# Performance work log

Hardware: AMD Instinct MI355X
Metric: run time of the kernel (lower is better)

The kernel has to match this reference:

```python
import jax, jax.numpy as jnp
import numpy as np

B = 256          # block_size
IN_BLOCKS = 16
OUT_BLOCKS = 16
BATCH, SEQ = 4, 2048


def setup_inputs() -> dict:
    key = jax.random.key(0)
    k1, k2, k3 = jax.random.split(key, 3)
    x = jax.random.normal(k1, (BATCH, SEQ, IN_BLOCKS * B), dtype=jnp.float32)
    c = jax.random.normal(k2, (OUT_BLOCKS, IN_BLOCKS, B), dtype=jnp.float32) * 0.01
    bias = jnp.zeros((OUT_BLOCKS * B,), dtype=jnp.float32)
    return {"x": x, "c": c, "bias": bias}


def reference(x, c, bias):
    # x: (batch, seq, in_features); c: (J, I, B); bias: (J*B,)
    batch, seq, in_f = x.shape
    J, I, Bsz = c.shape
    x_blocks = x.reshape(batch * seq, I, Bsz)            # (N, I, B)
    # FFT in float32 (matches circulant_matvec_fft internals)
    fft_c = jnp.fft.rfft(c.astype(jnp.float32), axis=-1)         # (J, I, F)
    fft_x = jnp.fft.rfft(x_blocks.astype(jnp.float32), axis=-1)  # (N, I, F)
    # y[n,j] = sum_i C_{j,i} x[n,i]  -> frequency-domain multiply + reduce over i
    fft_y = jnp.einsum('jif,nif->njf', fft_c, fft_x)              # (N, J, F)
    y_blocks = jnp.fft.irfft(fft_y, n=Bsz, axis=-1)               # (N, J, B)
    y = y_blocks.reshape(batch * seq, J * Bsz).astype(x.dtype) + bias
    return y.reshape(batch, seq, J * Bsz)
```

## Files before the change

kernel.cpp:

```cpp
#include <hip/hip_runtime.h>

typedef unsigned int uint;
typedef unsigned short ushort;
typedef __attribute__((ext_vector_type(8))) short  short8;
typedef __attribute__((ext_vector_type(8))) unsigned short u16x8;
typedef __attribute__((ext_vector_type(4))) float  f32x4;

__device__ __forceinline__ ushort f2b(float f) {
    uint u = __float_as_uint(f);
    u += 0x7FFFu + ((u >> 16) & 1u);
    return (ushort)(u >> 16);
}

__device__ __forceinline__ void async16(const void* g, void* l) {
    __builtin_amdgcn_global_load_lds(
        (const __attribute__((address_space(1))) void*)g,
        (__attribute__((address_space(3))) void*)l,
        16, 0, 0);
}

__global__ __launch_bounds__(256) void expand_w(const float* __restrict__ c,
                                                ushort* __restrict__ Wt) {
    const int j = blockIdx.x >> 4;
    const int i = blockIdx.x & 15;
    __shared__ ushort crev2[512];
    const float* cs = c + (size_t)(j * 16 + i) * 256;
    const int t = threadIdx.x;
    {
        ushort b = f2b(cs[(256 - t) & 255]);
        crev2[t] = b;
        crev2[t + 256] = b;
    }
    __syncthreads();
    const int tr = t >> 5;
    const int tm = (t & 31) * 8;
    for (int rb = 0; rb < 256; rb += 8) {
        const int k = rb + tr;
        u16x8 v;
#pragma unroll
        for (int u = 0; u < 8; ++u) v[u] = crev2[tm + u - k + 256];
        *(u16x8*)&Wt[(size_t)(j * 256 + k) * 4096 + i * 256 + tm] = v;
    }
}

__global__ __launch_bounds__(256) void conv_x(const float4* __restrict__ x,
                                              u16x8* __restrict__ xb, int n8) {
    int idx = blockIdx.x * blockDim.x + threadIdx.x;
    const int stride = gridDim.x * blockDim.x;
    for (; idx < n8; idx += stride) {
        float4 a = x[idx * 2];
        float4 b = x[idx * 2 + 1];
        u16x8 o;
        o[0] = f2b(a.x); o[1] = f2b(a.y); o[2] = f2b(a.z); o[3] = f2b(a.w);
        o[4] = f2b(b.x); o[5] = f2b(b.y); o[6] = f2b(b.z); o[7] = f2b(b.w);
        xb[idx] = o;
    }
}

#define BAR()   __builtin_amdgcn_s_barrier()
#define LGKM0() asm volatile("s_waitcnt lgkmcnt(0)" ::: "memory")
#define VMC6()  asm volatile("s_waitcnt vmcnt(6)" ::: "memory")
#define VMC0()  asm volatile("s_waitcnt vmcnt(0)" ::: "memory")
#define PRIO1() __builtin_amdgcn_s_setprio(1)
#define PRIO0() __builtin_amdgcn_s_setprio(0)

__global__ __launch_bounds__(512, 2) void gemm256(const ushort* __restrict__ A,
                                                  const ushort* __restrict__ Bt,
                                                  const float* __restrict__ bias,
                                                  float* __restrict__ C) {
    constexpr int K = 4096, N = 4096;
    __shared__ __align__(16) ushort lds[65536];

    const int tid  = threadIdx.x;
    const int wave = tid >> 6;
    const int lane = tid & 63;
    const int wr   = wave >> 2;
    const int wc   = wave & 3;
    const int lrow = lane & 15;
    const int kgrp = lane >> 4;

    const int wg  = (int)blockIdx.x;
    const int xcd = wg & 7;
    const int idx = wg >> 3;
    const int bm  = (xcd & 3) * 8 + (idx & 7);
    const int bn  = (xcd >> 2) * 8 + (idx >> 3);

    const int r0  = tid >> 3;
    const int cst = ((tid & 7) << 3) ^ ((r0 & 7) << 3);
    const ushort* gA  = A  + (size_t)(bm * 256 + r0) * K + cst;
    const ushort* gB  = Bt + (size_t)(bn * 256 + r0) * K + cst;
    const ushort* gA2 = gA + (size_t)128 * K;
    const ushort* gB2 = gB + (size_t)128 * K;
    const size_t r64 = (size_t)64 * K;

#define STAGE(buf, slot, src, kt) do {                          \
        ushort* d_ = &lds[(buf) * 32768 + (slot) * 8192 + tid * 8]; \
        async16((src) + (kt), d_);                              \
        async16((src) + r64 + (kt), d_ + 4096);                 \
    } while (0)

    const int swz = (lrow & 7) << 3;

    f32x4 acc[8][4];
#pragma unroll
    for (int m = 0; m < 8; ++m)
#pragma unroll
        for (int n = 0; n < 4; ++n) acc[m][n] = (f32x4){0.f, 0.f, 0.f, 0.f};

    short8 af[2][2], bf[4][2];

    auto LDAq = [&](int base, int qm) {
#pragma unroll
        for (int m = 0; m < 2; ++m) {
            const int mf = 2 * qm + m;
#pragma unroll
            for (int ks = 0; ks < 2; ++ks)
                af[m][ks] = *(const short8*)&lds[base + wr * 8192 +
                                                 (mf >> 2) * 4096 +
                                                 (mf & 3) * 1024 + lrow * 64 +
                                                 ((ks * 32 + kgrp * 8) ^ swz)];
        }
    };
    auto LDB = [&](int base) {
#pragma unroll
        for (int n = 0; n < 4; ++n)
#pragma unroll
            for (int ks = 0; ks < 2; ++ks)
                bf[n][ks] = *(const short8*)&lds[base + (2 + (wc >> 1)) * 8192 +
                                                 (wc & 1) * 4096 +
                                                 n * 1024 + lrow * 64 +
                                                 ((ks * 32 + kgrp * 8) ^ swz)];
    };

#define MMQ(QM) do {                                                         \
        _Pragma("unroll")                                                    \
        for (int m_ = 0; m_ < 2; ++m_)                                       \
            _Pragma("unroll")                                                \
            for (int n_ = 0; n_ < 4; ++n_)                                   \
                _Pragma("unroll")                                            \
                for (int ks_ = 0; ks_ < 2; ++ks_)                            \
                    acc[2 * (QM) + m_][n_] =                                 \
                        __builtin_amdgcn_mfma_f32_16x16x32_bf16(             \
                            af[m_][ks_], bf[n_][ks_],                        \
                            acc[2 * (QM) + m_][n_], 0, 0, 0);                \
    } while (0)

    STAGE(0, 2, gB, 0);  STAGE(0, 3, gB2, 0);  STAGE(0, 0, gA, 0);  STAGE(0, 1, gA2, 0);
    STAGE(1, 2, gB, 64); STAGE(1, 3, gB2, 64); STAGE(1, 0, gA, 64);
    VMC6();
    BAR();

    for (int it = 0; it < 31; ++it) {
        const int kt2 = it * 128 + 128, kt3 = kt2 + 64, ktn = kt2 - 64;
        LDB(0); LDAq(0, 0);
        STAGE(1, 1, gA2, ktn);
        BAR(); LGKM0(); PRIO1(); MMQ(0); PRIO0(); BAR();
        LDAq(0, 1);
        STAGE(0, 2, gB, kt2);
        BAR(); LGKM0(); PRIO1(); MMQ(1); PRIO0(); BAR();
        LDAq(0, 2);
        STAGE(0, 3, gB2, kt2);
        BAR(); LGKM0(); PRIO1(); MMQ(2); PRIO0(); BAR();
        LDAq(0, 3);
        STAGE(0, 0, gA, kt2);
        VMC6();
        BAR(); LGKM0(); PRIO1(); MMQ(3); PRIO0(); BAR();
        LDB(32768); LDAq(32768, 0);
        STAGE(0, 1, gA2, kt2);
        BAR(); LGKM0(); PRIO1(); MMQ(0); PRIO0(); BAR();
        LDAq(32768, 1);
        STAGE(1, 2, gB, kt3);
        BAR(); LGKM0(); PRIO1(); MMQ(1); PRIO0(); BAR();
        LDAq(32768, 2);
        STAGE(1, 3, gB2, kt3);
        BAR(); LGKM0(); PRIO1(); MMQ(2); PRIO0(); BAR();
        LDAq(32768, 3);
        STAGE(1, 0, gA, kt3);
        VMC6();
        BAR(); LGKM0(); PRIO1(); MMQ(3); PRIO0(); BAR();
    }

    {
        LDB(0); LDAq(0, 0);
        STAGE(1, 1, gA2, 4032);
        BAR(); LGKM0(); PRIO1(); MMQ(0); PRIO0(); BAR();
        LDAq(0, 1);
        BAR(); LGKM0(); PRIO1(); MMQ(1); PRIO0(); BAR();
        LDAq(0, 2);
        BAR(); LGKM0(); PRIO1(); MMQ(2); PRIO0(); BAR();
        LDAq(0, 3);
        VMC0();
        BAR(); LGKM0(); PRIO1(); MMQ(3); PRIO0(); BAR();
        LDB(32768); LDAq(32768, 0);
        LGKM0(); PRIO1(); MMQ(0); PRIO0();
        LDAq(32768, 1);
        LGKM0(); PRIO1(); MMQ(1); PRIO0();
        LDAq(32768, 2);
        LGKM0(); PRIO1(); MMQ(2); PRIO0();
        LDAq(32768, 3);
        LGKM0(); PRIO1(); MMQ(3); PRIO0();
    }

    const int colbase = bn * 256 + wc * 64 + lrow;
    float bv[4];
#pragma unroll
    for (int n = 0; n < 4; ++n) bv[n] = bias[colbase + n * 16];
    const int rowbase = bm * 256 + wr * 128 + kgrp * 4;
#pragma unroll
    for (int m = 0; m < 8; ++m)
#pragma unroll
        for (int n = 0; n < 4; ++n) {
            const size_t base = (size_t)(rowbase + m * 16) * N + colbase + n * 16;
#pragma unroll
            for (int r = 0; r < 4; ++r)
                C[base + (size_t)r * N] = acc[m][n][r] + bv[n];
        }
#undef STAGE
#undef MMQ
}

extern "C" void kernel_launch(void* const* d_in, const int* in_sizes, int n_in,
                              void* d_out, int out_size, void* d_ws, size_t ws_size,
                              hipStream_t stream) {
    const float* x    = (const float*)d_in[0];
    const float* c    = (const float*)d_in[1];
    const float* bias = (const float*)d_in[2];
    float* out = (float*)d_out;

    ushort* Wb = (ushort*)d_ws;
    ushort* Xb = Wb + (size_t)4096 * 4096;

    hipLaunchKernelGGL(expand_w, dim3(256), dim3(256), 0, stream, c, Wb);
    hipLaunchKernelGGL(conv_x, dim3(2048), dim3(256), 0, stream,
                       (const float4*)x, (u16x8*)Xb, 33554432 / 8);
    hipLaunchKernelGGL(gemm256, dim3(512), dim3(512), 0, stream,
                       Xb, Wb, bias, out);
}
```

Measured before the change: 270.9 us.

## Double-buffer LDS fragment registers to overlap ds_reads with MFMA quarters

Splits the A and B fragment registers into current and next sets, so the LDS reads for the next MFMA quarter are issued before the current quarter's MFMAs run. Waits relax from lgkmcnt(0) to lgkmcnt(4), letting those reads stay in flight during compute, and the next buffer's B fragments are prefetched at the buffer switch. The goal is to hide LDS read latency inside the MFMA stream. The cost is more VGPRs for the extra fragments, which could cause spills or hurt occupancy under launch_bounds(512,2), and the hand-counted waitcnt values must match the actual number of outstanding loads.

```diff
diff --git a/kernel.cpp b/kernel.cpp
--- a/kernel.cpp
+++ b/kernel.cpp
@@ -59,6 +59,7 @@
 
 #define BAR()   __builtin_amdgcn_s_barrier()
 #define LGKM0() asm volatile("s_waitcnt lgkmcnt(0)" ::: "memory")
+#define LGKM4() asm volatile("s_waitcnt lgkmcnt(4)" ::: "memory")
 #define VMC6()  asm volatile("s_waitcnt vmcnt(6)" ::: "memory")
 #define VMC0()  asm volatile("s_waitcnt vmcnt(0)" ::: "memory")
 #define PRIO1() __builtin_amdgcn_s_setprio(1)
@@ -107,32 +108,32 @@
 #pragma unroll
         for (int n = 0; n < 4; ++n) acc[m][n] = (f32x4){0.f, 0.f, 0.f, 0.f};
 
-    short8 af[2][2], bf[4][2];
-
-    auto LDAq = [&](int base, int qm) {
-#pragma unroll
-        for (int m = 0; m < 2; ++m) {
-            const int mf = 2 * qm + m;
-#pragma unroll
-            for (int ks = 0; ks < 2; ++ks)
-                af[m][ks] = *(const short8*)&lds[base + wr * 8192 +
-                                                 (mf >> 2) * 4096 +
-                                                 (mf & 3) * 1024 + lrow * 64 +
-                                                 ((ks * 32 + kgrp * 8) ^ swz)];
-        }
-    };
-    auto LDB = [&](int base) {
-#pragma unroll
-        for (int n = 0; n < 4; ++n)
-#pragma unroll
-            for (int ks = 0; ks < 2; ++ks)
-                bf[n][ks] = *(const short8*)&lds[base + (2 + (wc >> 1)) * 8192 +
-                                                 (wc & 1) * 4096 +
-                                                 n * 1024 + lrow * 64 +
-                                                 ((ks * 32 + kgrp * 8) ^ swz)];
-    };
-
-#define MMQ(QM) do {                                                         \
+    short8 afc[2][2], afn[2][2], bfc[4][2], bfn[4][2];
+
+#define LDAQ(dst, base, qm) do {                                             \
+        _Pragma("unroll")                                                    \
+        for (int m_ = 0; m_ < 2; ++m_) {                                     \
+            const int mf_ = 2 * (qm) + m_;                                   \
+            _Pragma("unroll")                                                \
+            for (int ks_ = 0; ks_ < 2; ++ks_)                                \
+                dst[m_][ks_] = *(const short8*)&lds[(base) + wr * 8192 +     \
+                    (mf_ >> 2) * 4096 + (mf_ & 3) * 1024 + lrow * 64 +       \
+                    ((ks_ * 32 + kgrp * 8) ^ swz)];                          \
+        }                                                                    \
+    } while (0)
+
+#define LDBQ(dst, base) do {                                                 \
+        _Pragma("unroll")                                                    \
+        for (int n_ = 0; n_ < 4; ++n_)                                       \
+            _Pragma("unroll")                                                \
+            for (int ks_ = 0; ks_ < 2; ++ks_)                                \
+                dst[n_][ks_] = *(const short8*)&lds[(base) +                 \
+                    (2 + (wc >> 1)) * 8192 + (wc & 1) * 4096 +               \
+                    n_ * 1024 + lrow * 64 +                                  \
+                    ((ks_ * 32 + kgrp * 8) ^ swz)];                          \
+    } while (0)
+
+#define MMQ(QM, AF, BF) do {                                                 \
         _Pragma("unroll")                                                    \
         for (int m_ = 0; m_ < 2; ++m_)                                       \
             _Pragma("unroll")                                                \
@@ -141,7 +142,7 @@
                 for (int ks_ = 0; ks_ < 2; ++ks_)                            \
                     acc[2 * (QM) + m_][n_] =                                 \
                         __builtin_amdgcn_mfma_f32_16x16x32_bf16(             \
-                            af[m_][ks_], bf[n_][ks_],                        \
+                            AF[m_][ks_], BF[n_][ks_],                        \
                             acc[2 * (QM) + m_][n_], 0, 0, 0);                \
     } while (0)
 
@@ -149,56 +150,59 @@
     STAGE(1, 2, gB, 64); STAGE(1, 3, gB2, 64); STAGE(1, 0, gA, 64);
     VMC6();
     BAR();
+    LDBQ(bfc, 0); LDAQ(afc, 0, 0);
 
     for (int it = 0; it < 31; ++it) {
         const int kt2 = it * 128 + 128, kt3 = kt2 + 64, ktn = kt2 - 64;
-        LDB(0); LDAq(0, 0);
+        LDAQ(afn, 0, 1);
         STAGE(1, 1, gA2, ktn);
-        BAR(); LGKM0(); PRIO1(); MMQ(0); PRIO0(); BAR();
-        LDAq(0, 1);
+        BAR(); LGKM4(); PRIO1(); MMQ(0, afc, bfc); PRIO0(); BAR();
+        LDAQ(afc, 0, 2);
         STAGE(0, 2, gB, kt2);
-        BAR(); LGKM0(); PRIO1(); MMQ(1); PRIO0(); BAR();
-        LDAq(0, 2);
+        BAR(); LGKM4(); PRIO1(); MMQ(1, afn, bfc); PRIO0(); BAR();
+        LDAQ(afn, 0, 3);
         STAGE(0, 3, gB2, kt2);
-        BAR(); LGKM0(); PRIO1(); MMQ(2); PRIO0(); BAR();
-        LDAq(0, 3);
+        BAR(); LGKM4(); PRIO1(); MMQ(2, afc, bfc); PRIO0(); BAR();
         STAGE(0, 0, gA, kt2);
         VMC6();
-        BAR(); LGKM0(); PRIO1(); MMQ(3); PRIO0(); BAR();
-        LDB(32768); LDAq(32768, 0);
+        BAR(); LGKM0();
+        LDBQ(bfn, 32768); LDAQ(afc, 32768, 0);
+        PRIO1(); MMQ(3, afn, bfc); PRIO0(); BAR();
+        LDAQ(afn, 32768, 1);
         STAGE(0, 1, gA2, kt2);
-        BAR(); LGKM0(); PRIO1(); MMQ(0); PRIO0(); BAR();
-        LDAq(32768, 1);
+        BAR(); LGKM4(); PRIO1(); MMQ(0, afc, bfn); PRIO0(); BAR();
+        LDAQ(afc, 32768, 2);
         STAGE(1, 2, gB, kt3);
-        BAR(); LGKM0(); PRIO1(); MMQ(1); PRIO0(); BAR();
-        LDAq(32768, 2);
+        BAR(); LGKM4(); PRIO1(); MMQ(1, afn, bfn); PRIO0(); BAR();
+        LDAQ(afn, 32768, 3);
         STAGE(1, 3, gB2, kt3);
-        BAR(); LGKM0(); PRIO1(); MMQ(2); PRIO0(); BAR();
-        LDAq(32768, 3);
+        BAR(); LGKM4(); PRIO1(); MMQ(2, afc, bfn); PRIO0(); BAR();
         STAGE(1, 0, gA, kt3);
         VMC6();
-        BAR(); LGKM0(); PRIO1(); MMQ(3); PRIO0(); BAR();
+        BAR(); LGKM0();
+        LDBQ(bfc, 0); LDAQ(afc, 0, 0);
+        PRIO1(); MMQ(3, afn, bfn); PRIO0(); BAR();
     }
 
     {
-        LDB(0); LDAq(0, 0);
+        LDAQ(afn, 0, 1);
         STAGE(1, 1, gA2, 4032);
-        BAR(); LGKM0(); PRIO1(); MMQ(0); PRIO0(); BAR();
-        LDAq(0, 1);
-        BAR(); LGKM0(); PRIO1(); MMQ(1); PRIO0(); BAR();
-        LDAq(0, 2);
-        BAR(); LGKM0(); PRIO1(); MMQ(2); PRIO0(); BAR();
-        LDAq(0, 3);
+        BAR(); LGKM4(); PRIO1(); MMQ(0, afc, bfc); PRIO0(); BAR();
+        LDAQ(afc, 0, 2);
+        BAR(); LGKM4(); PRIO1(); MMQ(1, afn, bfc); PRIO0(); BAR();
+        LDAQ(afn, 0, 3);
+        BAR(); LGKM4(); PRIO1(); MMQ(2, afc, bfc); PRIO0(); BAR();
         VMC0();
-        BAR(); LGKM0(); PRIO1(); MMQ(3); PRIO0(); BAR();
-        LDB(32768); LDAq(32768, 0);
-        LGKM0(); PRIO1(); MMQ(0); PRIO0();
-        LDAq(32768, 1);
-        LGKM0(); PRIO1(); MMQ(1); PRIO0();
-        LDAq(32768, 2);
-        LGKM0(); PRIO1(); MMQ(2); PRIO0();
-        LDAq(32768, 3);
-        LGKM0(); PRIO1(); MMQ(3); PRIO0();
+        BAR(); LGKM0();
+        LDBQ(bfn, 32768); LDAQ(afc, 32768, 0);
+        PRIO1(); MMQ(3, afn, bfc); PRIO0(); BAR();
+        LDAQ(afn, 32768, 1);
+        LGKM4(); PRIO1(); MMQ(0, afc, bfn); PRIO0();
+        LDAQ(afc, 32768, 2);
+        LGKM4(); PRIO1(); MMQ(1, afn, bfn); PRIO0();
+        LDAQ(afn, 32768, 3);
+        LGKM4(); PRIO1(); MMQ(2, afc, bfn); PRIO0();
+        LGKM0(); PRIO1(); MMQ(3, afn, bfn); PRIO0();
     }
 
     const int colbase = bn * 256 + wc * 64 + lrow;
@@ -216,6 +220,8 @@
                 C[base + (size_t)r * N] = acc[m][n][r] + bv[n];
         }
 #undef STAGE
+#undef LDAQ
+#undef LDBQ
 #undef MMQ
 }
 
```

After: 283.5 us. 4.7% more time.
